# Performance work log

Measured on AMD Instinct MI355X. Metric: run time of the kernel, lower is better.

The kernel has to match this reference:

```python
import jax, jax.numpy as jnp
import numpy as np

BATCH, N, NX, NU, NY = 64, 4096, 128, 32, 32


def setup_inputs() -> dict:
    key = jax.random.key(0)
    k1, k2, k3, k4, k5 = jax.random.split(key, 5)
    # A scaled to spectral radius ~0.9 so the recurrence is stable (module has is_stable()).
    A = jax.random.normal(k1, (NX, NX), jnp.float32) * (0.9 / np.sqrt(NX).astype(np.float32))
    B = jax.random.normal(k2, (NX, NU), jnp.float32) * (1.0 / np.sqrt(NU).astype(np.float32))
    C = jax.random.normal(k3, (NY, NX), jnp.float32) * (1.0 / np.sqrt(NX).astype(np.float32))
    D = jax.random.normal(k4, (NY, NU), jnp.float32) * (1.0 / np.sqrt(NU).astype(np.float32))
    d = jax.random.normal(k5, (BATCH, N, NU, 1), jnp.float32)
    return {"d": d, "A": A, "B": B, "C": C, "D": D}


def reference(d, A, B, C, D):
    # d: [batch, N, nu, 1]. LTI recurrence: x_{k+1} = A x_k + B u_k ; y_k = C x_k + D u_k, x_0 = 0.
    u = jnp.swapaxes(d[..., 0], 0, 1)  # [N, batch, nu] time-major for scan
    x0 = jnp.zeros((d.shape[0], A.shape[0]), d.dtype)  # [batch, nx]

    def step(x, uk):
        y = x @ C.T + uk @ D.T          # [batch, ny] uses pre-update state x_k
        x_next = x @ A.T + uk @ B.T     # [batch, nx]
        return x_next, (y, x)

    xN, (ys, xs) = jax.lax.scan(step, x0, u)
    y = jnp.swapaxes(ys, 0, 1)[..., None]                      # [batch, N, ny, 1]
    x = jnp.swapaxes(xs, 0, 1)                                 # [batch, N, nx] = x_0..x_{N-1}
    x = jnp.concatenate([x, xN[:, None]], axis=1)[..., None]   # [batch, N+1, nx, 1]
    return y, (x,)
```

## Files before the change

kernel.cpp:

```cpp
#include <hip/hip_runtime.h>
#include <stdint.h>
#include <stddef.h>

typedef short s8v   __attribute__((ext_vector_type(8)));
typedef float f32x4 __attribute__((ext_vector_type(4)));

union BF8 { s8v v; unsigned short u[8]; };

__device__ __forceinline__ unsigned short bf16_rn(float x) {
  unsigned u = __builtin_bit_cast(unsigned, x);
  u += 0x7FFFu + ((u >> 16) & 1u);
  return (unsigned short)(u >> 16);
}
__device__ __forceinline__ float bf16_f(unsigned short h) {
  unsigned u = ((unsigned)h) << 16;
  return __builtin_bit_cast(float, u);
}
__device__ __forceinline__ void split_f32(float x, unsigned short &h, unsigned short &l) {
  unsigned short hs = bf16_rn(x);
  h = hs;
  l = bf16_rn(x - bf16_f(hs));
}
__device__ __forceinline__ f32x4 mfma16(s8v a, s8v b, f32x4 c) {
  return __builtin_amdgcn_mfma_f32_16x16x32_bf16(a, b, c, 0, 0, 0);
}
__device__ __forceinline__ s8v cvt8(const float* p) {
  BF8 r;
  f32x4 x0 = *(const f32x4*)p, x1 = *(const f32x4*)(p + 4);
  #pragma unroll
  for (int i = 0; i < 4; ++i) { r.u[i] = bf16_rn(x0[i]); r.u[4 + i] = bf16_rn(x1[i]); }
  return r.v;
}

#define BATCH 64
#define NN    4096
#define NX    128
#define NU    32
#define NY    32

#define OFF_AH 0
#define OFF_AL 32768
#define OFF_BH 65536
#define OFF_BL 73728
#define OFF_CH 81920
#define OFF_CL 90112
#define OFF_DH 98304
#define OFF_DL 100352
#define OFF_GH 102400
#define OFF_GL 135168
#define OFF_P0 167936
#define OFF_P1 233472
#define OFF_V  299008
#define OFF_S  2396160
#define OFF_G2H 4493312
#define OFF_G2L 4526080
#define OFF_G3H 4558848
#define OFF_G3L 4591616
#define OFF_P2  4624384

__global__ void k_convert(const float* __restrict__ A, const float* __restrict__ B,
                          const float* __restrict__ C, const float* __restrict__ D,
                          unsigned short* Ah, unsigned short* Al,
                          unsigned short* Bh, unsigned short* Bl,
                          unsigned short* Ch, unsigned short* Cl,
                          unsigned short* Dh, unsigned short* Dl) {
  int idx = blockIdx.x * 256 + threadIdx.x;
  unsigned short h, l;
  if (idx < 16384)      { split_f32(A[idx], h, l); Ah[idx] = h; Al[idx] = l; }
  else if (idx < 20480) { int i = idx - 16384; split_f32(B[i], h, l); Bh[i] = h; Bl[i] = l; }
  else if (idx < 24576) { int i = idx - 20480; split_f32(C[i], h, l); Ch[i] = h; Cl[i] = l; }
  else if (idx < 25600) { int i = idx - 24576; split_f32(D[i], h, l); Dh[i] = h; Dl[i] = l; }
}

__global__ void k_mm128(const float* __restrict__ X, const float* __restrict__ Y,
                        float* __restrict__ Z, unsigned short* Zh, unsigned short* Zl,
                        int writeBF) {
  int gid = blockIdx.x * 256 + threadIdx.x;
  int row = gid >> 7, col = gid & 127;
  const float* xr = X + row * 128;
  float acc = 0.f;
  #pragma unroll 8
  for (int k = 0; k < 128; ++k) acc = fmaf(xr[k], Y[k * 128 + col], acc);
  Z[gid] = acc;
  if (writeBF) { unsigned short h, l; split_f32(acc, h, l); Zh[gid] = h; Zl[gid] = l; }
}

__global__ __launch_bounds__(256) void k_pass1(
    const float* __restrict__ d,
    const unsigned short* __restrict__ Ah, const unsigned short* __restrict__ Al,
    const unsigned short* __restrict__ Bh, const unsigned short* __restrict__ Bl,
    float* __restrict__ vout) {
  __shared__ unsigned short Xh[2][16][136];
  __shared__ unsigned short Xl[2][16][136];
  const int tid = threadIdx.x;
  const int w = tid >> 6, l = tid & 63, q = l >> 4, m = l & 15;
  const int g = blockIdx.x;

  s8v fAh[2][4], fAl[2][4], fBh[2], fBl[2];
  #pragma unroll
  for (int t2 = 0; t2 < 2; ++t2) {
    const int n = (2 * w + t2) * 16 + m;
    #pragma unroll
    for (int kt = 0; kt < 4; ++kt) {
      const int k0 = kt * 32 + q * 8;
      fAh[t2][kt] = *(const s8v*)(Ah + n * 128 + k0);
      fAl[t2][kt] = *(const s8v*)(Al + n * 128 + k0);
    }
    fBh[t2] = *(const s8v*)(Bh + n * 32 + q * 8);
    fBl[t2] = *(const s8v*)(Bl + n * 32 + q * 8);
  }
  for (int i = tid; i < 16 * 136; i += 256) {
    ((unsigned short*)Xh[0])[i] = 0;
    ((unsigned short*)Xl[0])[i] = 0;
  }
  __syncthreads();

  const int ch = g * 16 + m, b = ch >> 6, chunk = ch & 63;
  const float* ubase = d + ((size_t)b * NN + chunk * 64) * NU + q * 8;

  f32x4 cu0 = *(const f32x4*)ubase;
  f32x4 cu1 = *(const f32x4*)(ubase + 4);

  #pragma unroll 2
  for (int j = 0; j < 64; ++j) {
    const int p = j & 1;
    f32x4 nu0 = cu0, nu1 = cu1;
    if (j < 63) {
      const float* up = ubase + (size_t)(j + 1) * NU;
      nu0 = *(const f32x4*)up;
      nu1 = *(const f32x4*)(up + 4);
    }
    BF8 uh, ul;
    #pragma unroll
    for (int i = 0; i < 4; ++i) { split_f32(cu0[i], uh.u[i], ul.u[i]); split_f32(cu1[i], uh.u[4 + i], ul.u[4 + i]); }
    s8v fXh[4], fXl[4];
    #pragma unroll
    for (int kt = 0; kt < 4; ++kt) {
      fXh[kt] = *(const s8v*)&Xh[p][m][kt * 32 + q * 8];
      fXl[kt] = *(const s8v*)&Xl[p][m][kt * 32 + q * 8];
    }
    f32x4 acc[2];
    #pragma unroll
    for (int t2 = 0; t2 < 2; ++t2) {
      f32x4 a0 = {0.f,0.f,0.f,0.f}, a1 = {0.f,0.f,0.f,0.f}, a2 = {0.f,0.f,0.f,0.f};
      #pragma unroll
      for (int kt = 0; kt < 4; ++kt) a0 = mfma16(fXh[kt], fAh[t2][kt], a0);
      a0 = mfma16(uh.v, fBh[t2], a0);
      #pragma unroll
      for (int kt = 0; kt < 4; ++kt) a1 = mfma16(fXl[kt], fAh[t2][kt], a1);
      a1 = mfma16(ul.v, fBh[t2], a1);
      #pragma unroll
      for (int kt = 0; kt < 4; ++kt) a2 = mfma16(fXh[kt], fAl[t2][kt], a2);
      a2 = mfma16(uh.v, fBl[t2], a2);
      acc[t2] = a0 + a1 + a2;
    }
    #pragma unroll
    for (int t2 = 0; t2 < 2; ++t2) {
      const int col = (2 * w + t2) * 16 + m;
      #pragma unroll
      for (int r = 0; r < 4; ++r) {
        unsigned short h, lo;
        split_f32(acc[t2][r], h, lo);
        Xh[1 - p][q * 4 + r][col] = h;
        Xl[1 - p][q * 4 + r][col] = lo;
      }
    }
    __syncthreads();
    cu0 = nu0; cu1 = nu1;
  }
  const int lb = tid >> 4, i0 = (tid & 15) * 8;
  BF8 hh, ll;
  hh.v = *(const s8v*)&Xh[0][lb][i0];
  ll.v = *(const s8v*)&Xl[0][lb][i0];
  f32x4 o0, o1;
  #pragma unroll
  for (int i = 0; i < 4; ++i) { o0[i] = bf16_f(hh.u[i]) + bf16_f(ll.u[i]); o1[i] = bf16_f(hh.u[4 + i]) + bf16_f(ll.u[4 + i]); }
  float* vp = vout + ((size_t)(g * 16 + lb)) * 128 + i0;
  *(f32x4*)vp = o0;
  *(f32x4*)(vp + 4) = o1;
}

__global__ __launch_bounds__(256) void k_carry2(
    const unsigned short* __restrict__ Gh, const unsigned short* __restrict__ G2h,
    const unsigned short* __restrict__ G3h,
    const float* __restrict__ v, float* __restrict__ sout) {
  const int tid = threadIdx.x;
  const int w = tid >> 6, l = tid & 63, q = l >> 4, m = l & 15;
  const int g = blockIdx.x;

  s8v f1[2][4], f2[2][4], f3[2][4];
  #pragma unroll
  for (int t2 = 0; t2 < 2; ++t2) {
    const int n = (2 * w + t2) * 16 + m;
    #pragma unroll
    for (int kt = 0; kt < 4; ++kt) {
      const int k0 = kt * 32 + q * 8;
      f1[t2][kt] = *(const s8v*)(Gh  + n * 128 + k0);
      f2[t2][kt] = *(const s8v*)(G2h + n * 128 + k0);
      f3[t2][kt] = *(const s8v*)(G3h + n * 128 + k0);
    }
  }
  const int ch = g * 16 + m, c = ch & 63;
  const s8v zero = {0,0,0,0,0,0,0,0};
  s8v a2f[4], a3f[4], a4f[4];
  #pragma unroll
  for (int kt = 0; kt < 4; ++kt) {
    const int k0 = kt * 32 + q * 8;
    a2f[kt] = (c >= 2) ? cvt8(v + (size_t)(ch - 2) * 128 + k0) : zero;
    a3f[kt] = (c >= 3) ? cvt8(v + (size_t)(ch - 3) * 128 + k0) : zero;
    a4f[kt] = (c >= 4) ? cvt8(v + (size_t)(ch - 4) * 128 + k0) : zero;
  }
  f32x4 acc[2];
  #pragma unroll
  for (int t2 = 0; t2 < 2; ++t2) {
    f32x4 a = {0.f,0.f,0.f,0.f};
    #pragma unroll
    for (int kt = 0; kt < 4; ++kt) {
      a = mfma16(a2f[kt], f1[t2][kt], a);
      a = mfma16(a3f[kt], f2[t2][kt], a);
      a = mfma16(a4f[kt], f3[t2][kt], a);
    }
    acc[t2] = a;
  }
  #pragma unroll
  for (int t2 = 0; t2 < 2; ++t2) {
    #pragma unroll
    for (int r = 0; r < 4; ++r) {
      const int row = q * 4 + r, chr = g * 16 + row, cr = chr & 63;
      const int col = (2 * w + t2) * 16 + m;
      float sval = 0.f;
      if (cr >= 1) sval = acc[t2][r] + v[(size_t)(chr - 1) * 128 + col];
      sout[(size_t)chr * 128 + col] = sval;
    }
  }
}

__global__ __launch_bounds__(256) void k_pass2(
    const float* __restrict__ d, const float* __restrict__ s,
    const unsigned short* __restrict__ Ah, const unsigned short* __restrict__ Al,
    const unsigned short* __restrict__ Bh, const unsigned short* __restrict__ Bl,
    const unsigned short* __restrict__ Ch, const unsigned short* __restrict__ Cl,
    const unsigned short* __restrict__ Dh, const unsigned short* __restrict__ Dl,
    float* __restrict__ yout, float* __restrict__ xout) {
  __shared__ unsigned short Xh[2][16][136];
  __shared__ unsigned short Xl[2][16][136];
  const int tid = threadIdx.x;
  const int w = tid >> 6, l = tid & 63, q = l >> 4, m = l & 15;
  const int g = blockIdx.x;

  s8v fAh[2][4], fAl[2][4], fBh[2], fBl[2];
  #pragma unroll
  for (int t2 = 0; t2 < 2; ++t2) {
    const int n = (2 * w + t2) * 16 + m;
    #pragma unroll
    for (int kt = 0; kt < 4; ++kt) {
      const int k0 = kt * 32 + q * 8;
      fAh[t2][kt] = *(const s8v*)(Ah + n * 128 + k0);
      fAl[t2][kt] = *(const s8v*)(Al + n * 128 + k0);
    }
    fBh[t2] = *(const s8v*)(Bh + n * 32 + q * 8);
    fBl[t2] = *(const s8v*)(Bl + n * 32 + q * 8);
  }
  s8v fCh[4], fCl[4], fDh, fDl;
  {
    const int o = (w & 1) * 16 + m;
    #pragma unroll
    for (int kt = 0; kt < 4; ++kt) {
      const int k0 = kt * 32 + q * 8;
      fCh[kt] = *(const s8v*)(Ch + o * 128 + k0);
      fCl[kt] = *(const s8v*)(Cl + o * 128 + k0);
    }
    fDh = *(const s8v*)(Dh + o * 32 + q * 8);
    fDl = *(const s8v*)(Dl + o * 32 + q * 8);
  }

  const int lb = tid >> 4, i0 = (tid & 15) * 8;
  {
    const float* sp = s + ((size_t)(g * 16 + lb)) * 128 + i0;
    BF8 hh, ll;
    #pragma unroll
    for (int i = 0; i < 8; ++i) split_f32(sp[i], hh.u[i], ll.u[i]);
    *(s8v*)&Xh[0][lb][i0] = hh.v;
    *(s8v*)&Xl[0][lb][i0] = ll.v;
  }
  __syncthreads();

  const int ch = g * 16 + m, b = ch >> 6, chunk = ch & 63;
  const float* ubase = d + ((size_t)b * NN + chunk * 64) * NU + q * 8;

  const int chS = g * 16 + lb, bS = chS >> 6, chunkS = chS & 63;
  float* xbase = xout + ((size_t)bS * (NN + 1) + (size_t)chunkS * 64) * NX + i0;

  f32x4 cu0 = *(const f32x4*)ubase;
  f32x4 cu1 = *(const f32x4*)(ubase + 4);

  #pragma unroll 2
  for (int j = 0; j < 64; ++j) {
    const int p = j & 1;
    f32x4 nu0 = cu0, nu1 = cu1;
    if (j < 63) {
      const float* up = ubase + (size_t)(j + 1) * NU;
      nu0 = *(const f32x4*)up;
      nu1 = *(const f32x4*)(up + 4);
    }
    BF8 uh, ul;
    #pragma unroll
    for (int i = 0; i < 4; ++i) { split_f32(cu0[i], uh.u[i], ul.u[i]); split_f32(cu1[i], uh.u[4 + i], ul.u[4 + i]); }

    s8v fXh[4], fXl[4];
    #pragma unroll
    for (int kt = 0; kt < 4; ++kt) {
      fXh[kt] = *(const s8v*)&Xh[p][m][kt * 32 + q * 8];
      fXl[kt] = *(const s8v*)&Xl[p][m][kt * 32 + q * 8];
    }

    {
      BF8 hh, ll;
      hh.v = *(const s8v*)&Xh[p][lb][i0];
      ll.v = *(const s8v*)&Xl[p][lb][i0];
      f32x4 o0, o1;
      #pragma unroll
      for (int i = 0; i < 4; ++i) { o0[i] = bf16_f(hh.u[i]) + bf16_f(ll.u[i]); o1[i] = bf16_f(hh.u[4 + i]) + bf16_f(ll.u[4 + i]); }
      *(f32x4*)(xbase + (size_t)j * NX) = o0;
      *(f32x4*)(xbase + (size_t)j * NX + 4) = o1;
    }

    f32x4 acc[2];
    #pragma unroll
    for (int t2 = 0; t2 < 2; ++t2) {
      f32x4 a0 = {0.f,0.f,0.f,0.f}, a1 = {0.f,0.f,0.f,0.f}, a2 = {0.f,0.f,0.f,0.f};
      #pragma unroll
      for (int kt = 0; kt < 4; ++kt) a0 = mfma16(fXh[kt], fAh[t2][kt], a0);
      a0 = mfma16(uh.v, fBh[t2], a0);
      #pragma unroll
      for (int kt = 0; kt < 4; ++kt) a1 = mfma16(fXl[kt], fAh[t2][kt], a1);
      a1 = mfma16(ul.v, fBh[t2], a1);
      #pragma unroll
      for (int kt = 0; kt < 4; ++kt) a2 = mfma16(fXh[kt], fAl[t2][kt], a2);
      a2 = mfma16(uh.v, fBl[t2], a2);
      acc[t2] = a0 + a1 + a2;
    }

    if (w < 2) {
      f32x4 b0 = {0.f,0.f,0.f,0.f}, b1 = {0.f,0.f,0.f,0.f}, b2 = {0.f,0.f,0.f,0.f};
      #pragma unroll
      for (int kt = 0; kt < 4; ++kt) b0 = mfma16(fXh[kt], fCh[kt], b0);
      b0 = mfma16(uh.v, fDh, b0);
      #pragma unroll
      for (int kt = 0; kt < 4; ++kt) b1 = mfma16(fXl[kt], fCh[kt], b1);
      b1 = mfma16(ul.v, fDh, b1);
      #pragma unroll
      for (int kt = 0; kt < 4; ++kt) b2 = mfma16(fXh[kt], fCl[kt], b2);
      b2 = mfma16(uh.v, fDl, b2);
      f32x4 ay = b0 + b1 + b2;
      #pragma unroll
      for (int r = 0; r < 4; ++r) {
        const int chY = g * 16 + q * 4 + r;
        const int bY = chY >> 6;
        const int kY = (chY & 63) * 64 + j;
        yout[((size_t)bY * NN + kY) * NY + w * 16 + m] = ay[r];
      }
    }
    #pragma unroll
    for (int t2 = 0; t2 < 2; ++t2) {
      const int col = (2 * w + t2) * 16 + m;
      #pragma unroll
      for (int r = 0; r < 4; ++r) {
        unsigned short h, lo;
        split_f32(acc[t2][r], h, lo);
        Xh[1 - p][q * 4 + r][col] = h;
        Xl[1 - p][q * 4 + r][col] = lo;
      }
    }
    __syncthreads();
    cu0 = nu0; cu1 = nu1;
  }
  if ((g & 3) == 3 && lb == 15) {
    BF8 hh, ll;
    hh.v = *(const s8v*)&Xh[0][15][i0];
    ll.v = *(const s8v*)&Xl[0][15][i0];
    f32x4 o0, o1;
    #pragma unroll
    for (int i = 0; i < 4; ++i) { o0[i] = bf16_f(hh.u[i]) + bf16_f(ll.u[i]); o1[i] = bf16_f(hh.u[4 + i]) + bf16_f(ll.u[4 + i]); }
    float* fp = xout + ((size_t)(g >> 2) * (NN + 1) + NN) * NX + i0;
    *(f32x4*)fp = o0;
    *(f32x4*)(fp + 4) = o1;
  }
}

extern "C" void kernel_launch(void* const* d_in, const int* in_sizes, int n_in,
                              void* d_out, int out_size, void* d_ws, size_t ws_size,
                              hipStream_t stream) {
  (void)in_sizes; (void)n_in; (void)out_size; (void)ws_size;
  const float* d = (const float*)d_in[0];
  const float* A = (const float*)d_in[1];
  const float* B = (const float*)d_in[2];
  const float* C = (const float*)d_in[3];
  const float* D = (const float*)d_in[4];

  char* ws = (char*)d_ws;
  unsigned short* Ah = (unsigned short*)(ws + OFF_AH);
  unsigned short* Al = (unsigned short*)(ws + OFF_AL);
  unsigned short* Bh = (unsigned short*)(ws + OFF_BH);
  unsigned short* Bl = (unsigned short*)(ws + OFF_BL);
  unsigned short* Chp = (unsigned short*)(ws + OFF_CH);
  unsigned short* Clp = (unsigned short*)(ws + OFF_CL);
  unsigned short* Dhp = (unsigned short*)(ws + OFF_DH);
  unsigned short* Dlp = (unsigned short*)(ws + OFF_DL);
  unsigned short* Gh  = (unsigned short*)(ws + OFF_GH);
  unsigned short* Gl  = (unsigned short*)(ws + OFF_GL);
  unsigned short* G2h = (unsigned short*)(ws + OFF_G2H);
  unsigned short* G2l = (unsigned short*)(ws + OFF_G2L);
  unsigned short* G3h = (unsigned short*)(ws + OFF_G3H);
  unsigned short* G3l = (unsigned short*)(ws + OFF_G3L);
  float* P0 = (float*)(ws + OFF_P0);
  float* P1 = (float*)(ws + OFF_P1);
  float* P2 = (float*)(ws + OFF_P2);
  float* V  = (float*)(ws + OFF_V);
  float* S  = (float*)(ws + OFF_S);

  float* yout = (float*)d_out;
  float* xout = yout + (size_t)BATCH * NN * NY;

  k_convert<<<100, 256, 0, stream>>>(A, B, C, D, Ah, Al, Bh, Bl, Chp, Clp, Dhp, Dlp);
  k_mm128<<<64, 256, 0, stream>>>(A,  A,  P0, nullptr, nullptr, 0);
  k_mm128<<<64, 256, 0, stream>>>(P0, P0, P1, nullptr, nullptr, 0);
  k_mm128<<<64, 256, 0, stream>>>(P1, P1, P0, nullptr, nullptr, 0);
  k_mm128<<<64, 256, 0, stream>>>(P0, P0, P1, nullptr, nullptr, 0);
  k_mm128<<<64, 256, 0, stream>>>(P1, P1, P0, nullptr, nullptr, 0);
  k_mm128<<<64, 256, 0, stream>>>(P0, P0, P1, Gh,  Gl,  1);
  k_mm128<<<64, 256, 0, stream>>>(P1, P1, P2, G2h, G2l, 1);
  k_mm128<<<64, 256, 0, stream>>>(P2, P1, P0, G3h, G3l, 1);

  k_pass1<<<256, 256, 0, stream>>>(d, Ah, Al, Bh, Bl, V);
  k_carry2<<<256, 256, 0, stream>>>(Gh, G2h, G3h, V, S);
  k_pass2<<<256, 256, 0, stream>>>(d, S, Ah, Al, Bh, Bl, Chp, Clp, Dhp, Dlp, yout, xout);
}
```

Measured before the change: 342.1 us.

## Advance recurrence two steps per iteration using A^2, AB, CA, CB

The chunked scan in pass1 and pass2 now advances the state two time steps per iteration using precomputed A², AB, CA and CB matrices. This halves the serial dependency chain and the number of block-wide barriers, at the cost of more MFMA work per iteration. The carry kernel drops the three-term G/G2/G3 correction for a single hi/lo split of G, and the matrix-power chain is shortened with the first squaring fused into the conversion kernel. Rounding for the bf16 hi/lo split becomes truncation, which makes the conversion cheaper but may change the numerical error.

```diff
diff --git a/kernel.cpp b/kernel.cpp
--- a/kernel.cpp
+++ b/kernel.cpp
@@ -2,34 +2,31 @@
 #include <stdint.h>
 #include <stddef.h>
 
+typedef unsigned short ushort_t;
 typedef short s8v   __attribute__((ext_vector_type(8)));
 typedef float f32x4 __attribute__((ext_vector_type(4)));
 
 union BF8 { s8v v; unsigned short u[8]; };
 
-__device__ __forceinline__ unsigned short bf16_rn(float x) {
-  unsigned u = __builtin_bit_cast(unsigned, x);
-  u += 0x7FFFu + ((u >> 16) & 1u);
-  return (unsigned short)(u >> 16);
-}
 __device__ __forceinline__ float bf16_f(unsigned short h) {
   unsigned u = ((unsigned)h) << 16;
   return __builtin_bit_cast(float, u);
 }
-__device__ __forceinline__ void split_f32(float x, unsigned short &h, unsigned short &l) {
-  unsigned short hs = bf16_rn(x);
-  h = hs;
-  l = bf16_rn(x - bf16_f(hs));
+__device__ __forceinline__ void split_trunc(float x, unsigned short &h, unsigned short &l) {
+  unsigned u = __builtin_bit_cast(unsigned, x);
+  h = (unsigned short)(u >> 16);
+  float hi = __builtin_bit_cast(float, u & 0xFFFF0000u);
+  float r = x - hi;
+  l = (unsigned short)(__builtin_bit_cast(unsigned, r) >> 16);
 }
 __device__ __forceinline__ f32x4 mfma16(s8v a, s8v b, f32x4 c) {
   return __builtin_amdgcn_mfma_f32_16x16x32_bf16(a, b, c, 0, 0, 0);
 }
-__device__ __forceinline__ s8v cvt8(const float* p) {
-  BF8 r;
-  f32x4 x0 = *(const f32x4*)p, x1 = *(const f32x4*)(p + 4);
-  #pragma unroll
-  for (int i = 0; i < 4; ++i) { r.u[i] = bf16_rn(x0[i]); r.u[4 + i] = bf16_rn(x1[i]); }
-  return r.v;
+__device__ __forceinline__ void split8(f32x4 a, f32x4 b, s8v &h, s8v &l) {
+  BF8 hh, ll;
+  #pragma unroll
+  for (int i = 0; i < 4; ++i) { split_trunc(a[i], hh.u[i], ll.u[i]); split_trunc(b[i], hh.u[4 + i], ll.u[4 + i]); }
+  h = hh.v; l = ll.v;
 }
 
 #define BATCH 64
@@ -37,39 +34,60 @@
 #define NX    128
 #define NU    32
 #define NY    32
-
-#define OFF_AH 0
-#define OFF_AL 32768
-#define OFF_BH 65536
-#define OFF_BL 73728
-#define OFF_CH 81920
-#define OFF_CL 90112
-#define OFF_DH 98304
-#define OFF_DL 100352
-#define OFF_GH 102400
-#define OFF_GL 135168
-#define OFF_P0 167936
-#define OFF_P1 233472
-#define OFF_V  299008
-#define OFF_S  2396160
-#define OFF_G2H 4493312
-#define OFF_G2L 4526080
-#define OFF_G3H 4558848
-#define OFF_G3L 4591616
-#define OFF_P2  4624384
-
-__global__ void k_convert(const float* __restrict__ A, const float* __restrict__ B,
+#define LPAD  132
+
+#define OFF_AH   0
+#define OFF_AL   32768
+#define OFF_BH   65536
+#define OFF_BL   73728
+#define OFF_CH   81920
+#define OFF_CL   90112
+#define OFF_DH   98304
+#define OFF_DL   100352
+#define OFF_GH   102400
+#define OFF_GL   135168
+#define OFF_P0   167936
+#define OFF_P1   233472
+#define OFF_V    299008
+#define OFF_S    2396160
+#define OFF_A2H  4493312
+#define OFF_A2L  4526080
+#define OFF_ABH  4558848
+#define OFF_ABL  4567040
+#define OFF_CAH  4575232
+#define OFF_CAL  4583424
+#define OFF_CBH  4591616
+#define OFF_CBL  4593664
+
+__global__ void k_mm_conv(const float* __restrict__ A, const float* __restrict__ B,
                           const float* __restrict__ C, const float* __restrict__ D,
+                          float* __restrict__ P, unsigned short* A2h, unsigned short* A2l,
                           unsigned short* Ah, unsigned short* Al,
                           unsigned short* Bh, unsigned short* Bl,
                           unsigned short* Ch, unsigned short* Cl,
                           unsigned short* Dh, unsigned short* Dl) {
-  int idx = blockIdx.x * 256 + threadIdx.x;
-  unsigned short h, l;
-  if (idx < 16384)      { split_f32(A[idx], h, l); Ah[idx] = h; Al[idx] = l; }
-  else if (idx < 20480) { int i = idx - 16384; split_f32(B[i], h, l); Bh[i] = h; Bl[i] = l; }
-  else if (idx < 24576) { int i = idx - 20480; split_f32(C[i], h, l); Ch[i] = h; Cl[i] = l; }
-  else if (idx < 25600) { int i = idx - 24576; split_f32(D[i], h, l); Dh[i] = h; Dl[i] = l; }
+  int gid = blockIdx.x * 256 + threadIdx.x;
+  if (blockIdx.x < 64) {
+    int row = gid >> 7, col = gid & 127;
+    const float* xr = A + row * 128;
+    float a0 = 0.f, a1 = 0.f;
+    #pragma unroll 8
+    for (int k = 0; k < 128; k += 2) {
+      a0 = fmaf(xr[k],     A[k * 128 + col],       a0);
+      a1 = fmaf(xr[k + 1], A[(k + 1) * 128 + col], a1);
+    }
+    float acc = a0 + a1;
+    P[gid] = acc;
+    unsigned short h, l; split_trunc(acc, h, l);
+    A2h[gid] = h; A2l[gid] = l;
+  } else {
+    int idx = gid - 16384;
+    unsigned short h, l;
+    if (idx < 16384)      { split_trunc(A[idx], h, l); Ah[idx] = h; Al[idx] = l; }
+    else if (idx < 20480) { int i = idx - 16384; split_trunc(B[i], h, l); Bh[i] = h; Bl[i] = l; }
+    else if (idx < 24576) { int i = idx - 20480; split_trunc(C[i], h, l); Ch[i] = h; Cl[i] = l; }
+    else if (idx < 25600) { int i = idx - 24576; split_trunc(D[i], h, l); Dh[i] = h; Dl[i] = l; }
+  }
 }
 
 __global__ void k_mm128(const float* __restrict__ X, const float* __restrict__ Y,
@@ -78,38 +96,71 @@
   int gid = blockIdx.x * 256 + threadIdx.x;
   int row = gid >> 7, col = gid & 127;
   const float* xr = X + row * 128;
+  float a0 = 0.f, a1 = 0.f;
+  #pragma unroll 8
+  for (int k = 0; k < 128; k += 2) {
+    a0 = fmaf(xr[k],     Y[k * 128 + col],       a0);
+    a1 = fmaf(xr[k + 1], Y[(k + 1) * 128 + col], a1);
+  }
+  float acc = a0 + a1;
+  Z[gid] = acc;
+  if (writeBF) { unsigned short h, l; split_trunc(acc, h, l); Zh[gid] = h; Zl[gid] = l; }
+}
+
+__global__ void k_misc(const float* __restrict__ A, const float* __restrict__ B,
+                       const float* __restrict__ C,
+                       unsigned short* ABh, unsigned short* ABl,
+                       unsigned short* CAh, unsigned short* CAl,
+                       unsigned short* CBh, unsigned short* CBl) {
+  int gid = blockIdx.x * 256 + threadIdx.x;
   float acc = 0.f;
-  #pragma unroll 8
-  for (int k = 0; k < 128; ++k) acc = fmaf(xr[k], Y[k * 128 + col], acc);
-  Z[gid] = acc;
-  if (writeBF) { unsigned short h, l; split_f32(acc, h, l); Zh[gid] = h; Zl[gid] = l; }
-}
-
-__global__ __launch_bounds__(256) void k_pass1(
+  unsigned short h, l;
+  if (gid < 4096) {
+    int row = gid >> 5, col = gid & 31;
+    #pragma unroll 8
+    for (int k = 0; k < 128; ++k) acc = fmaf(A[row * 128 + k], B[k * 32 + col], acc);
+    split_trunc(acc, h, l); ABh[gid] = h; ABl[gid] = l;
+  } else if (gid < 8192) {
+    int i = gid - 4096, row = i >> 7, col = i & 127;
+    #pragma unroll 8
+    for (int k = 0; k < 128; ++k) acc = fmaf(C[row * 128 + k], A[k * 128 + col], acc);
+    split_trunc(acc, h, l); CAh[i] = h; CAl[i] = l;
+  } else if (gid < 9216) {
+    int i = gid - 8192, row = i >> 5, col = i & 31;
+    #pragma unroll 8
+    for (int k = 0; k < 128; ++k) acc = fmaf(C[row * 128 + k], B[k * 32 + col], acc);
+    split_trunc(acc, h, l); CBh[i] = h; CBl[i] = l;
+  }
+}
+
+__global__ __launch_bounds__(256, 1) void k_pass1(
     const float* __restrict__ d,
-    const unsigned short* __restrict__ Ah, const unsigned short* __restrict__ Al,
-    const unsigned short* __restrict__ Bh, const unsigned short* __restrict__ Bl,
+    const unsigned short* __restrict__ A2h, const unsigned short* __restrict__ A2l,
+    const unsigned short* __restrict__ ABh, const unsigned short* __restrict__ ABl,
+    const unsigned short* __restrict__ Bh,  const unsigned short* __restrict__ Bl,
     float* __restrict__ vout) {
-  __shared__ unsigned short Xh[2][16][136];
-  __shared__ unsigned short Xl[2][16][136];
+  __shared__ unsigned short Xh[2][16][LPAD];
+  __shared__ unsigned short Xl[2][16][LPAD];
   const int tid = threadIdx.x;
   const int w = tid >> 6, l = tid & 63, q = l >> 4, m = l & 15;
   const int g = blockIdx.x;
 
-  s8v fAh[2][4], fAl[2][4], fBh[2], fBl[2];
+  s8v fA2h[2][4], fA2l[2][4], fABh[2], fABl[2], fBh[2], fBl[2];
   #pragma unroll
   for (int t2 = 0; t2 < 2; ++t2) {
     const int n = (2 * w + t2) * 16 + m;
     #pragma unroll
     for (int kt = 0; kt < 4; ++kt) {
       const int k0 = kt * 32 + q * 8;
-      fAh[t2][kt] = *(const s8v*)(Ah + n * 128 + k0);
-      fAl[t2][kt] = *(const s8v*)(Al + n * 128 + k0);
-    }
-    fBh[t2] = *(const s8v*)(Bh + n * 32 + q * 8);
-    fBl[t2] = *(const s8v*)(Bl + n * 32 + q * 8);
-  }
-  for (int i = tid; i < 16 * 136; i += 256) {
+      fA2h[t2][kt] = *(const s8v*)(A2h + n * 128 + k0);
+      fA2l[t2][kt] = *(const s8v*)(A2l + n * 128 + k0);
+    }
+    fABh[t2] = *(const s8v*)(ABh + n * 32 + q * 8);
+    fABl[t2] = *(const s8v*)(ABl + n * 32 + q * 8);
+    fBh[t2]  = *(const s8v*)(Bh  + n * 32 + q * 8);
+    fBl[t2]  = *(const s8v*)(Bl  + n * 32 + q * 8);
+  }
+  for (int i = tid; i < 16 * LPAD; i += 256) {
     ((unsigned short*)Xh[0])[i] = 0;
     ((unsigned short*)Xl[0])[i] = 0;
   }
@@ -118,97 +169,100 @@
   const int ch = g * 16 + m, b = ch >> 6, chunk = ch & 63;
   const float* ubase = d + ((size_t)b * NN + chunk * 64) * NU + q * 8;
 
-  f32x4 cu0 = *(const f32x4*)ubase;
-  f32x4 cu1 = *(const f32x4*)(ubase + 4);
-
+  f32x4 cu[4];
+  cu[0] = *(const f32x4*)(ubase);      cu[1] = *(const f32x4*)(ubase + 4);
+  cu[2] = *(const f32x4*)(ubase + 32); cu[3] = *(const f32x4*)(ubase + 36);
+
+  f32x4 acc[2];
   #pragma unroll 2
-  for (int j = 0; j < 64; ++j) {
-    const int p = j & 1;
-    f32x4 nu0 = cu0, nu1 = cu1;
-    if (j < 63) {
-      const float* up = ubase + (size_t)(j + 1) * NU;
-      nu0 = *(const f32x4*)up;
-      nu1 = *(const f32x4*)(up + 4);
-    }
-    BF8 uh, ul;
-    #pragma unroll
-    for (int i = 0; i < 4; ++i) { split_f32(cu0[i], uh.u[i], ul.u[i]); split_f32(cu1[i], uh.u[4 + i], ul.u[4 + i]); }
+  for (int r = 0; r < 32; ++r) {
+    const int p = r & 1;
+    f32x4 nu0 = cu[0], nu1 = cu[1], nu2 = cu[2], nu3 = cu[3];
+    if (r < 31) {
+      const float* up = ubase + (size_t)(2 * r + 2) * NU;
+      nu0 = *(const f32x4*)up;        nu1 = *(const f32x4*)(up + 4);
+      nu2 = *(const f32x4*)(up + 32); nu3 = *(const f32x4*)(up + 36);
+    }
+    s8v u0h, u0l, u1h, u1l;
+    split8(cu[0], cu[1], u0h, u0l);
+    split8(cu[2], cu[3], u1h, u1l);
     s8v fXh[4], fXl[4];
     #pragma unroll
     for (int kt = 0; kt < 4; ++kt) {
       fXh[kt] = *(const s8v*)&Xh[p][m][kt * 32 + q * 8];
       fXl[kt] = *(const s8v*)&Xl[p][m][kt * 32 + q * 8];
     }
-    f32x4 acc[2];
     #pragma unroll
     for (int t2 = 0; t2 < 2; ++t2) {
       f32x4 a0 = {0.f,0.f,0.f,0.f}, a1 = {0.f,0.f,0.f,0.f}, a2 = {0.f,0.f,0.f,0.f};
       #pragma unroll
-      for (int kt = 0; kt < 4; ++kt) a0 = mfma16(fXh[kt], fAh[t2][kt], a0);
-      a0 = mfma16(uh.v, fBh[t2], a0);
-      #pragma unroll
-      for (int kt = 0; kt < 4; ++kt) a1 = mfma16(fXl[kt], fAh[t2][kt], a1);
-      a1 = mfma16(ul.v, fBh[t2], a1);
-      #pragma unroll
-      for (int kt = 0; kt < 4; ++kt) a2 = mfma16(fXh[kt], fAl[t2][kt], a2);
-      a2 = mfma16(uh.v, fBl[t2], a2);
+      for (int kt = 0; kt < 4; ++kt) a0 = mfma16(fXh[kt], fA2h[t2][kt], a0);
+      a0 = mfma16(u0h, fABh[t2], a0);
+      a0 = mfma16(u1h, fBh[t2],  a0);
+      #pragma unroll
+      for (int kt = 0; kt < 4; ++kt) a1 = mfma16(fXl[kt], fA2h[t2][kt], a1);
+      a1 = mfma16(u0l, fABh[t2], a1);
+      a1 = mfma16(u1l, fBh[t2],  a1);
+      #pragma unroll
+      for (int kt = 0; kt < 4; ++kt) a2 = mfma16(fXh[kt], fA2l[t2][kt], a2);
+      a2 = mfma16(u0h, fABl[t2], a2);
+      a2 = mfma16(u1h, fBl[t2],  a2);
       acc[t2] = a0 + a1 + a2;
     }
-    #pragma unroll
-    for (int t2 = 0; t2 < 2; ++t2) {
-      const int col = (2 * w + t2) * 16 + m;
-      #pragma unroll
-      for (int r = 0; r < 4; ++r) {
-        unsigned short h, lo;
-        split_f32(acc[t2][r], h, lo);
-        Xh[1 - p][q * 4 + r][col] = h;
-        Xl[1 - p][q * 4 + r][col] = lo;
+    if (r < 31) {
+      #pragma unroll
+      for (int t2 = 0; t2 < 2; ++t2) {
+        const int col = (2 * w + t2) * 16 + m;
+        #pragma unroll
+        for (int rr = 0; rr < 4; ++rr) {
+          unsigned short h, lo;
+          split_trunc(acc[t2][rr], h, lo);
+          Xh[1 - p][q * 4 + rr][col] = h;
+          Xl[1 - p][q * 4 + rr][col] = lo;
+        }
       }
-    }
-    __syncthreads();
-    cu0 = nu0; cu1 = nu1;
-  }
-  const int lb = tid >> 4, i0 = (tid & 15) * 8;
-  BF8 hh, ll;
-  hh.v = *(const s8v*)&Xh[0][lb][i0];
-  ll.v = *(const s8v*)&Xl[0][lb][i0];
-  f32x4 o0, o1;
-  #pragma unroll
-  for (int i = 0; i < 4; ++i) { o0[i] = bf16_f(hh.u[i]) + bf16_f(ll.u[i]); o1[i] = bf16_f(hh.u[4 + i]) + bf16_f(ll.u[4 + i]); }
-  float* vp = vout + ((size_t)(g * 16 + lb)) * 128 + i0;
-  *(f32x4*)vp = o0;
-  *(f32x4*)(vp + 4) = o1;
-}
-
-__global__ __launch_bounds__(256) void k_carry2(
-    const unsigned short* __restrict__ Gh, const unsigned short* __restrict__ G2h,
-    const unsigned short* __restrict__ G3h,
+      __syncthreads();
+      cu[0] = nu0; cu[1] = nu1; cu[2] = nu2; cu[3] = nu3;
+    }
+  }
+  #pragma unroll
+  for (int t2 = 0; t2 < 2; ++t2) {
+    const int col = (2 * w + t2) * 16 + m;
+    #pragma unroll
+    for (int rr = 0; rr < 4; ++rr) {
+      const int row = g * 16 + q * 4 + rr;
+      vout[(size_t)row * 128 + col] = acc[t2][rr];
+    }
+  }
+}
+
+__global__ __launch_bounds__(256, 1) void k_carry(
+    const unsigned short* __restrict__ Gh, const unsigned short* __restrict__ Gl,
     const float* __restrict__ v, float* __restrict__ sout) {
   const int tid = threadIdx.x;
   const int w = tid >> 6, l = tid & 63, q = l >> 4, m = l & 15;
   const int g = blockIdx.x;
 
-  s8v f1[2][4], f2[2][4], f3[2][4];
+  s8v fGh[2][4], fGl[2][4];
   #pragma unroll
   for (int t2 = 0; t2 < 2; ++t2) {
     const int n = (2 * w + t2) * 16 + m;
     #pragma unroll
     for (int kt = 0; kt < 4; ++kt) {
       const int k0 = kt * 32 + q * 8;
-      f1[t2][kt] = *(const s8v*)(Gh  + n * 128 + k0);
-      f2[t2][kt] = *(const s8v*)(G2h + n * 128 + k0);
-      f3[t2][kt] = *(const s8v*)(G3h + n * 128 + k0);
-    }
-  }
-  const int ch = g * 16 + m, c = ch & 63;
+      fGh[t2][kt] = *(const s8v*)(Gh + n * 128 + k0);
+      fGl[t2][kt] = *(const s8v*)(Gl + n * 128 + k0);
+    }
+  }
+  const int chm = g * 16 + m, cm = chm & 63;
   const s8v zero = {0,0,0,0,0,0,0,0};
-  s8v a2f[4], a3f[4], a4f[4];
+  s8v v2h[4], v2l[4];
   #pragma unroll
   for (int kt = 0; kt < 4; ++kt) {
-    const int k0 = kt * 32 + q * 8;
-    a2f[kt] = (c >= 2) ? cvt8(v + (size_t)(ch - 2) * 128 + k0) : zero;
-    a3f[kt] = (c >= 3) ? cvt8(v + (size_t)(ch - 3) * 128 + k0) : zero;
-    a4f[kt] = (c >= 4) ? cvt8(v + (size_t)(ch - 4) * 128 + k0) : zero;
+    if (cm >= 2) {
+      const float* vp = v + (size_t)(chm - 2) * 128 + kt * 32 + q * 8;
+      split8(*(const f32x4*)vp, *(const f32x4*)(vp + 4), v2h[kt], v2l[kt]);
+    } else { v2h[kt] = zero; v2l[kt] = zero; }
   }
   f32x4 acc[2];
   #pragma unroll
@@ -216,97 +270,131 @@
     f32x4 a = {0.f,0.f,0.f,0.f};
     #pragma unroll
     for (int kt = 0; kt < 4; ++kt) {
-      a = mfma16(a2f[kt], f1[t2][kt], a);
-      a = mfma16(a3f[kt], f2[t2][kt], a);
-      a = mfma16(a4f[kt], f3[t2][kt], a);
+      a = mfma16(v2h[kt], fGh[t2][kt], a);
+      a = mfma16(v2l[kt], fGh[t2][kt], a);
+      a = mfma16(v2h[kt], fGl[t2][kt], a);
     }
     acc[t2] = a;
   }
   #pragma unroll
   for (int t2 = 0; t2 < 2; ++t2) {
-    #pragma unroll
-    for (int r = 0; r < 4; ++r) {
-      const int row = q * 4 + r, chr = g * 16 + row, cr = chr & 63;
-      const int col = (2 * w + t2) * 16 + m;
-      float sval = 0.f;
-      if (cr >= 1) sval = acc[t2][r] + v[(size_t)(chr - 1) * 128 + col];
-      sout[(size_t)chr * 128 + col] = sval;
-    }
-  }
-}
-
-__global__ __launch_bounds__(256) void k_pass2(
+    const int col = (2 * w + t2) * 16 + m;
+    #pragma unroll
+    for (int rr = 0; rr < 4; ++rr) {
+      const int chr = g * 16 + q * 4 + rr, cr = chr & 63;
+      float sv = 0.f;
+      if (cr >= 1) sv = acc[t2][rr] + v[(size_t)(chr - 1) * 128 + col];
+      sout[(size_t)chr * 128 + col] = sv;
+    }
+  }
+}
+
+__global__ __launch_bounds__(256, 1) void k_pass2(
     const float* __restrict__ d, const float* __restrict__ s,
-    const unsigned short* __restrict__ Ah, const unsigned short* __restrict__ Al,
-    const unsigned short* __restrict__ Bh, const unsigned short* __restrict__ Bl,
-    const unsigned short* __restrict__ Ch, const unsigned short* __restrict__ Cl,
-    const unsigned short* __restrict__ Dh, const unsigned short* __restrict__ Dl,
+    const unsigned short* __restrict__ Ah,  const unsigned short* __restrict__ Al,
+    const unsigned short* __restrict__ A2h, const unsigned short* __restrict__ A2l,
+    const unsigned short* __restrict__ ABh, const unsigned short* __restrict__ ABl,
+    const unsigned short* __restrict__ Bh,  const unsigned short* __restrict__ Bl,
+    const unsigned short* __restrict__ Ch,  const unsigned short* __restrict__ Cl,
+    const unsigned short* __restrict__ CAh, const unsigned short* __restrict__ CAl,
+    const unsigned short* __restrict__ CBh, const unsigned short* __restrict__ CBl,
+    const unsigned short* __restrict__ Dh,  const unsigned short* __restrict__ Dl,
     float* __restrict__ yout, float* __restrict__ xout) {
-  __shared__ unsigned short Xh[2][16][136];
-  __shared__ unsigned short Xl[2][16][136];
+  __shared__ unsigned short Xh[2][16][LPAD];
+  __shared__ unsigned short Xl[2][16][LPAD];
   const int tid = threadIdx.x;
   const int w = tid >> 6, l = tid & 63, q = l >> 4, m = l & 15;
   const int g = blockIdx.x;
 
-  s8v fAh[2][4], fAl[2][4], fBh[2], fBl[2];
+  s8v fAh[2][4], fAl[2][4], fA2h[2][4], fA2l[2][4];
+  s8v fABh[2], fABl[2], fBh[2], fBl[2];
   #pragma unroll
   for (int t2 = 0; t2 < 2; ++t2) {
     const int n = (2 * w + t2) * 16 + m;
     #pragma unroll
     for (int kt = 0; kt < 4; ++kt) {
       const int k0 = kt * 32 + q * 8;
-      fAh[t2][kt] = *(const s8v*)(Ah + n * 128 + k0);
-      fAl[t2][kt] = *(const s8v*)(Al + n * 128 + k0);
-    }
-    fBh[t2] = *(const s8v*)(Bh + n * 32 + q * 8);
-    fBl[t2] = *(const s8v*)(Bl + n * 32 + q * 8);
-  }
-  s8v fCh[4], fCl[4], fDh, fDl;
+      fAh[t2][kt]  = *(const s8v*)(Ah  + n * 128 + k0);
+      fAl[t2][kt]  = *(const s8v*)(Al  + n * 128 + k0);
+      fA2h[t2][kt] = *(const s8v*)(A2h + n * 128 + k0);
+      fA2l[t2][kt] = *(const s8v*)(A2l + n * 128 + k0);
+    }
+    fABh[t2] = *(const s8v*)(ABh + n * 32 + q * 8);
+    fABl[t2] = *(const s8v*)(ABl + n * 32 + q * 8);
+    fBh[t2]  = *(const s8v*)(Bh  + n * 32 + q * 8);
+    fBl[t2]  = *(const s8v*)(Bl  + n * 32 + q * 8);
+  }
+  s8v fCh[4] = {}, fCl[4] = {}, fCAh[4] = {}, fCAl[4] = {};
+  s8v fCBh = {}, fCBl = {}, fDh = {}, fDl = {};
+  if (w < 2) {
+    const int o = w * 16 + m;
+    #pragma unroll
+    for (int kt = 0; kt < 4; ++kt) {
+      const int k0 = kt * 32 + q * 8;
+      fCh[kt]  = *(const s8v*)(Ch  + o * 128 + k0);
+      fCl[kt]  = *(const s8v*)(Cl  + o * 128 + k0);
+      fCAh[kt] = *(const s8v*)(CAh + o * 128 + k0);
+      fCAl[kt] = *(const s8v*)(CAl + o * 128 + k0);
+    }
+    fCBh = *(const s8v*)(CBh + o * 32 + q * 8);
+    fCBl = *(const s8v*)(CBl + o * 32 + q * 8);
+    fDh  = *(const s8v*)(Dh  + o * 32 + q * 8);
+    fDl  = *(const s8v*)(Dl  + o * 32 + q * 8);
+  }
+
   {
-    const int o = (w & 1) * 16 + m;
-    #pragma unroll
-    for (int kt = 0; kt < 4; ++kt) {
-      const int k0 = kt * 32 + q * 8;
-      fCh[kt] = *(const s8v*)(Ch + o * 128 + k0);
-      fCl[kt] = *(const s8v*)(Cl + o * 128 + k0);
-    }
-    fDh = *(const s8v*)(Dh + o * 32 + q * 8);
-    fDl = *(const s8v*)(Dl + o * 32 + q * 8);
-  }
-
-  const int lb = tid >> 4, i0 = (tid & 15) * 8;
-  {
-    const float* sp = s + ((size_t)(g * 16 + lb)) * 128 + i0;
-    BF8 hh, ll;
-    #pragma unroll
-    for (int i = 0; i < 8; ++i) split_f32(sp[i], hh.u[i], ll.u[i]);
-    *(s8v*)&Xh[0][lb][i0] = hh.v;
-    *(s8v*)&Xl[0][lb][i0] = ll.v;
+    const int lb = tid >> 4, i0 = (tid & 15) * 8;
+    const int chS = g * 16 + lb, bS = chS >> 6, cS = chS & 63;
+    const float* sp = s + (size_t)chS * 128 + i0;
+    f32x4 s0 = *(const f32x4*)sp, s1 = *(const f32x4*)(sp + 4);
+    s8v hh, ll;
+    split8(s0, s1, hh, ll);
+    *(s8v*)&Xh[0][lb][i0] = hh;
+    *(s8v*)&Xl[0][lb][i0] = ll;
+    float* xp = xout + ((size_t)bS * (NN + 1) + (size_t)cS * 64) * NX + i0;
+    *(f32x4*)xp = s0;
+    *(f32x4*)(xp + 4) = s1;
   }
   __syncthreads();
 
   const int ch = g * 16 + m, b = ch >> 6, chunk = ch & 63;
   const float* ubase = d + ((size_t)b * NN + chunk * 64) * NU + q * 8;
 
-  const int chS = g * 16 + lb, bS = chS >> 6, chunkS = chS & 63;
-  float* xbase = xout + ((size_t)bS * (NN + 1) + (size_t)chunkS * 64) * NX + i0;
-
-  f32x4 cu0 = *(const f32x4*)ubase;
-  f32x4 cu1 = *(const f32x4*)(ubase + 4);
+  float* xptr[2][4];
+  bool xlast[2][4];
+  float* yptr[4];
+  #pragma unroll
+  for (int t2 = 0; t2 < 2; ++t2) {
+    const int col = (2 * w + t2) * 16 + m;
+    #pragma unroll
+    for (int rr = 0; rr < 4; ++rr) {
+      const int chX = g * 16 + q * 4 + rr, bX = chX >> 6, cX = chX & 63;
+      xptr[t2][rr] = xout + ((size_t)bX * (NN + 1) + (size_t)cX * 64 + 1) * NX + col;
+      xlast[t2][rr] = (cX == 63);
+    }
+  }
+  #pragma unroll
+  for (int rr = 0; rr < 4; ++rr) {
+    const int chY = g * 16 + q * 4 + rr, bY = chY >> 6, cY = chY & 63;
+    yptr[rr] = yout + ((size_t)bY * NN + (size_t)cY * 64) * NY + w * 16 + m;
+  }
+
+  f32x4 cu[4];
+  cu[0] = *(const f32x4*)(ubase);      cu[1] = *(const f32x4*)(ubase + 4);
+  cu[2] = *(const f32x4*)(ubase + 32); cu[3] = *(const f32x4*)(ubase + 36);
 
   #pragma unroll 2
-  for (int j = 0; j < 64; ++j) {
-    const int p = j & 1;
-    f32x4 nu0 = cu0, nu1 = cu1;
-    if (j < 63) {
-      const float* up = ubase + (size_t)(j + 1) * NU;
-      nu0 = *(const f32x4*)up;
-      nu1 = *(const f32x4*)(up + 4);
-    }
-    BF8 uh, ul;
-    #pragma unroll
-    for (int i = 0; i < 4; ++i) { split_f32(cu0[i], uh.u[i], ul.u[i]); split_f32(cu1[i], uh.u[4 + i], ul.u[4 + i]); }
-
+  for (int r = 0; r < 32; ++r) {
+    const int p = r & 1;
+    f32x4 nu0 = cu[0], nu1 = cu[1], nu2 = cu[2], nu3 = cu[3];
+    if (r < 31) {
+      const float* up = ubase + (size_t)(2 * r + 2) * NU;
+      nu0 = *(const f32x4*)up;        nu1 = *(const f32x4*)(up + 4);
+      nu2 = *(const f32x4*)(up + 32); nu3 = *(const f32x4*)(up + 36);
+    }
+    s8v u0h, u0l, u1h, u1l;
+    split8(cu[0], cu[1], u0h, u0l);
+    split8(cu[2], cu[3], u1h, u1l);
     s8v fXh[4], fXl[4];
     #pragma unroll
     for (int kt = 0; kt < 4; ++kt) {
@@ -314,77 +402,105 @@
       fXl[kt] = *(const s8v*)&Xl[p][m][kt * 32 + q * 8];
     }
 
-    {
-      BF8 hh, ll;
-      hh.v = *(const s8v*)&Xh[p][lb][i0];
-      ll.v = *(const s8v*)&Xl[p][lb][i0];
-      f32x4 o0, o1;
-      #pragma unroll
-      for (int i = 0; i < 4; ++i) { o0[i] = bf16_f(hh.u[i]) + bf16_f(ll.u[i]); o1[i] = bf16_f(hh.u[4 + i]) + bf16_f(ll.u[4 + i]); }
-      *(f32x4*)(xbase + (size_t)j * NX) = o0;
-      *(f32x4*)(xbase + (size_t)j * NX + 4) = o1;
-    }
-
-    f32x4 acc[2];
+    f32x4 y1[2];
     #pragma unroll
     for (int t2 = 0; t2 < 2; ++t2) {
       f32x4 a0 = {0.f,0.f,0.f,0.f}, a1 = {0.f,0.f,0.f,0.f}, a2 = {0.f,0.f,0.f,0.f};
       #pragma unroll
       for (int kt = 0; kt < 4; ++kt) a0 = mfma16(fXh[kt], fAh[t2][kt], a0);
-      a0 = mfma16(uh.v, fBh[t2], a0);
+      a0 = mfma16(u0h, fBh[t2], a0);
       #pragma unroll
       for (int kt = 0; kt < 4; ++kt) a1 = mfma16(fXl[kt], fAh[t2][kt], a1);
-      a1 = mfma16(ul.v, fBh[t2], a1);
+      a1 = mfma16(u0l, fBh[t2], a1);
       #pragma unroll
       for (int kt = 0; kt < 4; ++kt) a2 = mfma16(fXh[kt], fAl[t2][kt], a2);
-      a2 = mfma16(uh.v, fBl[t2], a2);
+      a2 = mfma16(u0h, fBl[t2], a2);
+      y1[t2] = a0 + a1 + a2;
+    }
+    f32x4 acc[2];
+    #pragma unroll
+    for (int t2 = 0; t2 < 2; ++t2) {
+      f32x4 a0 = {0.f,0.f,0.f,0.f}, a1 = {0.f,0.f,0.f,0.f}, a2 = {0.f,0.f,0.f,0.f};
+      #pragma unroll
+      for (int kt = 0; kt < 4; ++kt) a0 = mfma16(fXh[kt], fA2h[t2][kt], a0);
+      a0 = mfma16(u0h, fABh[t2], a0);
+      a0 = mfma16(u1h, fBh[t2],  a0);
+      #pragma unroll
+      for (int kt = 0; kt < 4; ++kt) a1 = mfma16(fXl[kt], fA2h[t2][kt], a1);
+      a1 = mfma16(u0l, fABh[t2], a1);
+      a1 = mfma16(u1l, fBh[t2],  a1);
+      #pragma unroll
+      for (int kt = 0; kt < 4; ++kt) a2 = mfma16(fXh[kt], fA2l[t2][kt], a2);
+      a2 = mfma16(u0h, fABl[t2], a2);
+      a2 = mfma16(u1h, fBl[t2],  a2);
       acc[t2] = a0 + a1 + a2;
+    }
+
+    #pragma unroll
+    for (int t2 = 0; t2 < 2; ++t2) {
+      #pragma unroll
+      for (int rr = 0; rr < 4; ++rr) {
+        *(xptr[t2][rr]) = y1[t2][rr];
+        if (r < 31 || xlast[t2][rr]) *(xptr[t2][rr] + NX) = acc[t2][rr];
+      }
     }
 
     if (w < 2) {
       f32x4 b0 = {0.f,0.f,0.f,0.f}, b1 = {0.f,0.f,0.f,0.f}, b2 = {0.f,0.f,0.f,0.f};
       #pragma unroll
       for (int kt = 0; kt < 4; ++kt) b0 = mfma16(fXh[kt], fCh[kt], b0);
-      b0 = mfma16(uh.v, fDh, b0);
+      b0 = mfma16(u0h, fDh, b0);
       #pragma unroll
       for (int kt = 0; kt < 4; ++kt) b1 = mfma16(fXl[kt], fCh[kt], b1);
-      b1 = mfma16(ul.v, fDh, b1);
+      b1 = mfma16(u0l, fDh, b1);
       #pragma unroll
       for (int kt = 0; kt < 4; ++kt) b2 = mfma16(fXh[kt], fCl[kt], b2);
-      b2 = mfma16(uh.v, fDl, b2);
-      f32x4 ay = b0 + b1 + b2;
-      #pragma unroll
-      for (int r = 0; r < 4; ++r) {
-        const int chY = g * 16 + q * 4 + r;
-        const int bY = chY >> 6;
-        const int kY = (chY & 63) * 64 + j;
-        yout[((size_t)bY * NN + kY) * NY + w * 16 + m] = ay[r];
+      b2 = mfma16(u0h, fDl, b2);
+      f32x4 y0 = b0 + b1 + b2;
+
+      f32x4 c0 = {0.f,0.f,0.f,0.f}, c1 = {0.f,0.f,0.f,0.f}, c2 = {0.f,0.f,0.f,0.f};
+      #pragma unroll
+      for (int kt = 0; kt < 4; ++kt) c0 = mfma16(fXh[kt], fCAh[kt], c0);
+      c0 = mfma16(u0h, fCBh, c0);
+      c0 = mfma16(u1h, fDh,  c0);
+      #pragma unroll
+      for (int kt = 0; kt < 4; ++kt) c1 = mfma16(fXl[kt], fCAh[kt], c1);
+      c1 = mfma16(u0l, fCBh, c1);
+      c1 = mfma16(u1l, fDh,  c1);
+      #pragma unroll
+      for (int kt = 0; kt < 4; ++kt) c2 = mfma16(fXh[kt], fCAl[kt], c2);
+      c2 = mfma16(u0h, fCBl, c2);
+      c2 = mfma16(u1h, fDl,  c2);
+      f32x4 yo = c0 + c1 + c2;
+
+      #pragma unroll
+      for (int rr = 0; rr < 4; ++rr) {
+        *(yptr[rr]) = y0[rr];
+        *(yptr[rr] + NY) = yo[rr];
       }
     }
-    #pragma unroll
-    for (int t2 = 0; t2 < 2; ++t2) {
-      const int col = (2 * w + t2) * 16 + m;
-      #pragma unroll
-      for (int r = 0; r < 4; ++r) {
-        unsigned short h, lo;
-        split_f32(acc[t2][r], h, lo);
-        Xh[1 - p][q * 4 + r][col] = h;
-        Xl[1 - p][q * 4 + r][col] = lo;
+
+    if (r < 31) {
+      #pragma unroll
+      for (int t2 = 0; t2 < 2; ++t2) {
+        const int col = (2 * w + t2) * 16 + m;
+        #pragma unroll
+        for (int rr = 0; rr < 4; ++rr) {
+          unsigned short h, lo;
+          split_trunc(acc[t2][rr], h, lo);
+          Xh[1 - p][q * 4 + rr][col] = h;
+          Xl[1 - p][q * 4 + rr][col] = lo;
+        }
       }
-    }
-    __syncthreads();
-    cu0 = nu0; cu1 = nu1;
-  }
-  if ((g & 3) == 3 && lb == 15) {
-    BF8 hh, ll;
-    hh.v = *(const s8v*)&Xh[0][15][i0];
-    ll.v = *(const s8v*)&Xl[0][15][i0];
-    f32x4 o0, o1;
-    #pragma unroll
-    for (int i = 0; i < 4; ++i) { o0[i] = bf16_f(hh.u[i]) + bf16_f(ll.u[i]); o1[i] = bf16_f(hh.u[4 + i]) + bf16_f(ll.u[4 + i]); }
-    float* fp = xout + ((size_t)(g >> 2) * (NN + 1) + NN) * NX + i0;
-    *(f32x4*)fp = o0;
-    *(f32x4*)(fp + 4) = o1;
+      __syncthreads();
+      cu[0] = nu0; cu[1] = nu1; cu[2] = nu2; cu[3] = nu3;
+      #pragma unroll
+      for (int t2 = 0; t2 < 2; ++t2)
+        #pragma unroll
+        for (int rr = 0; rr < 4; ++rr) xptr[t2][rr] += 2 * NX;
+      #pragma unroll
+      for (int rr = 0; rr < 4; ++rr) yptr[rr] += 2 * NY;
+    }
   }
 }
 
@@ -399,40 +515,43 @@
   const float* D = (const float*)d_in[4];
 
   char* ws = (char*)d_ws;
-  unsigned short* Ah = (unsigned short*)(ws + OFF_AH);
-  unsigned short* Al = (unsigned short*)(ws + OFF_AL);
-  unsigned short* Bh = (unsigned short*)(ws + OFF_BH);
-  unsigned short* Bl = (unsigned short*)(ws + OFF_BL);
+  unsigned short* Ah  = (unsigned short*)(ws + OFF_AH);
+  unsigned short* Al  = (unsigned short*)(ws + OFF_AL);
+  unsigned short* Bh  = (unsigned short*)(ws + OFF_BH);
+  unsigned short* Bl  = (unsigned short*)(ws + OFF_BL);
   unsigned short* Chp = (unsigned short*)(ws + OFF_CH);
   unsigned short* Clp = (unsigned short*)(ws + OFF_CL);
   unsigned short* Dhp = (unsigned short*)(ws + OFF_DH);
   unsigned short* Dlp = (unsigned short*)(ws + OFF_DL);
   unsigned short* Gh  = (unsigned short*)(ws + OFF_GH);
   unsigned short* Gl  = (unsigned short*)(ws + OFF_GL);
-  unsigned short* G2h = (unsigned short*)(ws + OFF_G2H);
-  unsigned short* G2l = (unsigned short*)(ws + OFF_G2L);
-  unsigned short* G3h = (unsigned short*)(ws + OFF_G3H);
-  unsigned short* G3l = (unsigned short*)(ws + OFF_G3L);
+  unsigned short* A2h = (unsigned short*)(ws + OFF_A2H);
+  unsigned short* A2l = (unsigned short*)(ws + OFF_A2L);
+  unsigned short* ABh = (unsigned short*)(ws + OFF_ABH);
+  unsigned short* ABl = (unsigned short*)(ws + OFF_ABL);
+  unsigned short* CAh = (unsigned short*)(ws + OFF_CAH);
+  unsigned short* CAl = (unsigned short*)(ws + OFF_CAL);
+  unsigned short* CBh = (unsigned short*)(ws + OFF_CBH);
+  unsigned short* CBl = (unsigned short*)(ws + OFF_CBL);
   float* P0 = (float*)(ws + OFF_P0);
   float* P1 = (float*)(ws + OFF_P1);
-  float* P2 = (float*)(ws + OFF_P2);
   float* V  = (float*)(ws + OFF_V);
   float* S  = (float*)(ws + OFF_S);
 
   float* yout = (float*)d_out;
   float* xout = yout + (size_t)BATCH * NN * NY;
 
-  k_convert<<<100, 256, 0, stream>>>(A, B, C, D, Ah, Al, Bh, Bl, Chp, Clp, Dhp, Dlp);
-  k_mm128<<<64, 256, 0, stream>>>(A,  A,  P0, nullptr, nullptr, 0);
+  k_mm_conv<<<164, 256, 0, stream>>>(A, B, C, D, P0, A2h, A2l,
+                                     Ah, Al, Bh, Bl, Chp, Clp, Dhp, Dlp);
   k_mm128<<<64, 256, 0, stream>>>(P0, P0, P1, nullptr, nullptr, 0);
   k_mm128<<<64, 256, 0, stream>>>(P1, P1, P0, nullptr, nullptr, 0);
   k_mm128<<<64, 256, 0, stream>>>(P0, P0, P1, nullptr, nullptr, 0);
   k_mm128<<<64, 256, 0, stream>>>(P1, P1, P0, nullptr, nullptr, 0);
-  k_mm128<<<64, 256, 0, stream>>>(P0, P0, P1, Gh,  Gl,  1);
-  k_mm128<<<64, 256, 0, stream>>>(P1, P1, P2, G2h, G2l, 1);
-  k_mm128<<<64, 256, 0, stream>>>(P2, P1, P0, G3h, G3l, 1);
-
-  k_pass1<<<256, 256, 0, stream>>>(d, Ah, Al, Bh, Bl, V);
-  k_carry2<<<256, 256, 0, stream>>>(Gh, G2h, G3h, V, S);
-  k_pass2<<<256, 256, 0, stream>>>(d, S, Ah, Al, Bh, Bl, Chp, Clp, Dhp, Dlp, yout, xout);
-}
+  k_mm128<<<64, 256, 0, stream>>>(P0, P0, P1, Gh, Gl, 1);
+  k_misc<<<36, 256, 0, stream>>>(A, B, C, ABh, ABl, CAh, CAl, CBh, CBl);
+
+  k_pass1<<<256, 256, 0, stream>>>(d, A2h, A2l, ABh, ABl, Bh, Bl, V);
+  k_carry<<<256, 256, 0, stream>>>(Gh, Gl, V, S);
+  k_pass2<<<256, 256, 0, stream>>>(d, S, Ah, Al, A2h, A2l, ABh, ABl, Bh, Bl,
+                                   Chp, Clp, CAh, CAl, CBh, CBl, Dhp, Dlp, yout, xout);
+}
```

New measurement: 300.1 us. 12.3% less time.
